# Kernel optimization log

Hardware: AMD Instinct MI355X
Metric: run time of the kernel (lower is better)

The kernel has to match this reference:

```python
import jax, jax.numpy as jnp
import numpy as np

HIDDEN = 2048
INPUT = 2048
BATCH = 4096


def setup_inputs() -> dict:
    key = jax.random.key(0)
    ks = jax.random.split(key, 7)
    x = jax.random.normal(ks[0], (BATCH, INPUT), dtype=jnp.float32)
    h = jax.random.normal(ks[1], (BATCH, HIDDEN), dtype=jnp.float32)
    c = jax.random.normal(ks[2], (BATCH, HIDDEN), dtype=jnp.float32)
    # learned parameters (RandomNormal init stddev=0.05 analogue; scale irrelevant for correctness)
    w_ih = jax.random.normal(ks[3], (4, INPUT, HIDDEN), dtype=jnp.float32) * 0.05
    w_hh = jax.random.normal(ks[4], (4, HIDDEN, HIDDEN), dtype=jnp.float32) * 0.05
    b_ih = jax.random.normal(ks[5], (4, HIDDEN), dtype=jnp.float32) * 0.05
    b_hh = jax.random.normal(ks[6], (4, HIDDEN), dtype=jnp.float32) * 0.05
    return {"x": x, "h": h, "c": c, "w_ih": w_ih, "w_hh": w_hh, "b_ih": b_ih, "b_hh": b_hh}


def reference(x, h, c, w_ih, w_hh, b_ih, b_hh):
    # gates: [4, B, H] = x @ w_ih[g] and h @ w_hh[g], batched over gate dim g
    gates = (
        jnp.einsum("bi,gih->gbh", x, w_ih)
        + jnp.einsum("bh,ghk->gbk", h, w_hh)
        + (b_ih + b_hh)[:, None, :]
    )
    ingate = jax.nn.sigmoid(gates[0])
    forgetgate = jax.nn.sigmoid(gates[1])
    cellgate = jnp.tanh(gates[2])
    outgate = jax.nn.sigmoid(gates[3])
    c_new = forgetgate * c + ingate * cellgate
    h_new = outgate * jnp.tanh(c_new)
    return (h_new, c_new)
```

## Files before the change

### kernel.cpp

```cpp
#include <hip/hip_runtime.h>

#define BATCH  4096
#define HIDDEN 2048
#define INPUT  2048
#define KDIM   4096
#define NDIM   8192
#define BM 256
#define BN 256
#define BK 64
#define NT (KDIM / BK)

typedef __attribute__((ext_vector_type(8))) short short8;
typedef __attribute__((ext_vector_type(4))) float float4v;


__device__ __forceinline__ unsigned short f2bf(float f) {
    union { float f; unsigned u; } v; v.f = f;
    unsigned r = v.u + 0x7FFFu + ((v.u >> 16) & 1u);
    return (unsigned short)(r >> 16);
}

__device__ __forceinline__ void gl2lds16(const unsigned short* g, unsigned short* l) {
    __builtin_amdgcn_global_load_lds(
        (const __attribute__((address_space(1))) unsigned int*)g,
        (__attribute__((address_space(3))) unsigned int*)l,
        16, 0, 0);
}

__device__ __forceinline__ float sigm(float x) {
    return 1.0f / (1.0f + __expf(-x));
}
__device__ __forceinline__ float tanh_fast(float x) {
    return 2.0f / (1.0f + __expf(-2.0f * x)) - 1.0f;
}

__device__ __forceinline__ void fence_bar() {
    asm volatile("" ::: "memory");
    __builtin_amdgcn_s_barrier();
    asm volatile("" ::: "memory");
}


__global__ void pack_x_kernel(const float* __restrict__ x, const float* __restrict__ h,
                              unsigned short* __restrict__ Xb) {
    int idx = blockIdx.x * 256 + threadIdx.x;
    int b  = idx >> 9;
    int ko = idx & 511;
    const float* src = (ko < 256) ? (x + (size_t)b * INPUT  + (size_t)ko * 8)
                                  : (h + (size_t)b * HIDDEN + (size_t)(ko - 256) * 8);
    float4 v0 = *(const float4*)(src);
    float4 v1 = *(const float4*)(src + 4);
    union { unsigned short us[8]; uint4 v; } o;
    o.us[0] = f2bf(v0.x); o.us[1] = f2bf(v0.y); o.us[2] = f2bf(v0.z); o.us[3] = f2bf(v0.w);
    o.us[4] = f2bf(v1.x); o.us[5] = f2bf(v1.y); o.us[6] = f2bf(v1.z); o.us[7] = f2bf(v1.w);
    *(uint4*)(Xb + (size_t)b * KDIM + (size_t)ko * 8) = o.v;
}


__global__ void pack_w_kernel(const float* __restrict__ w_ih, const float* __restrict__ w_hh,
                              unsigned short* __restrict__ Wt) {
    __shared__ unsigned short tile[32][136];
    const int k0 = blockIdx.x * 128;
    const int j0 = blockIdx.y * 32;
    const int g  = blockIdx.z;
    const float* src = (k0 < INPUT)
        ? (w_ih + (size_t)g * INPUT  * HIDDEN + (size_t)k0 * HIDDEN + j0)
        : (w_hh + (size_t)g * HIDDEN * HIDDEN + (size_t)(k0 - INPUT) * HIDDEN + j0);

    const int tid = threadIdx.x;
    const int jl  = (tid & 7) * 4;
    const int kl  = (tid >> 3) * 2;
#pragma unroll
    for (int p = 0; p < 2; ++p) {
        const int k = kl + p * 64;
        float4 v0 = *(const float4*)(src + (size_t)k * HIDDEN + jl);
        float4 v1 = *(const float4*)(src + (size_t)(k + 1) * HIDDEN + jl);
        unsigned p0 = (unsigned)f2bf(v0.x) | ((unsigned)f2bf(v1.x) << 16);
        unsigned p1 = (unsigned)f2bf(v0.y) | ((unsigned)f2bf(v1.y) << 16);
        unsigned p2 = (unsigned)f2bf(v0.z) | ((unsigned)f2bf(v1.z) << 16);
        unsigned p3 = (unsigned)f2bf(v0.w) | ((unsigned)f2bf(v1.w) << 16);
        *(unsigned*)&tile[jl + 0][k] = p0;
        *(unsigned*)&tile[jl + 1][k] = p1;
        *(unsigned*)&tile[jl + 2][k] = p2;
        *(unsigned*)&tile[jl + 3][k] = p3;
    }
    __syncthreads();

#pragma unroll
    for (int p = 0; p < 2; ++p) {
        const int cch = tid + p * 256;
        const int j   = cch >> 4;
        const int k8  = cch & 15;
        uint4 v = *(const uint4*)&tile[j][k8 * 8];
        *(uint4*)(Wt + (size_t)(4 * (j0 + j) + g) * KDIM + k0 + k8 * 8) = v;
    }
}


__global__ __launch_bounds__(512, 2)
void gemm_kernel(const unsigned short* __restrict__ A,
                 const unsigned short* __restrict__ B,
                 const float* __restrict__ c,
                 const float* __restrict__ b_ih,
                 const float* __restrict__ b_hh,
                 float* __restrict__ out) {
    extern __shared__ unsigned short lds[];
    unsigned short* cA = lds;
    unsigned short* nA = lds + 16384;
    unsigned short* cB = lds + 32768;
    unsigned short* nB = lds + 49152;

    const int tid  = threadIdx.x;
    const int wid  = tid >> 6;
    const int lane = tid & 63;
    const int ln   = lane & 15;
    const int kq   = lane >> 4;
    const int wmr  = (wid >> 2) * 128;
    const int wnr  = (wid & 3) * 64;
    const int m0   = blockIdx.y * BM;
    const int n0   = blockIdx.x * BN;

    const int srow  = tid >> 3;
    const int scol8 = (tid & 7) ^ (srow & 7);
    const unsigned short* gA[4];
    const unsigned short* gB[4];
#pragma unroll
    for (int cN = 0; cN < 4; ++cN) {
        gA[cN] = A + (size_t)(m0 + cN * 64 + srow) * KDIM + scol8 * 8;
        gB[cN] = B + (size_t)(n0 + cN * 64 + srow) * KDIM + scol8 * 8;
    }
    const int dOff = tid * 8;

    const int abase = (wmr + ln) * 64;
    const int bbase = (wnr + ln) * 64;
    const int sk0 = ((0 + kq) ^ (ln & 7)) * 8;
    const int sk1 = ((4 + kq) ^ (ln & 7)) * 8;

    float4v acc[8][4];
#pragma unroll
    for (int i = 0; i < 8; ++i)
#pragma unroll
        for (int j = 0; j < 4; ++j)
            acc[i][j] = (float4v){0.f, 0.f, 0.f, 0.f};

#define STAGE_A(cN) gl2lds16(gA[cN] + konext, nA + (cN) * 4096 + dOff)
#define STAGE_B(cN) gl2lds16(gB[cN] + konext, nB + (cN) * 4096 + dOff)

    {
        const int konext = 0;
        unsigned short* sA = cA; unsigned short* sB = cB;
#pragma unroll
        for (int cN = 0; cN < 4; ++cN) gl2lds16(gB[cN], sB + cN * 4096 + dOff);
#pragma unroll
        for (int cN = 0; cN < 4; ++cN) gl2lds16(gA[cN], sA + cN * 4096 + dOff);
        (void)konext;
    }

    short8 bf[4][2];

    for (int T = 0; T < NT; ++T) {
        const bool last = (T == NT - 1);
        const int konext = (T + 1) * BK;

        if (!last) { STAGE_B(0); STAGE_B(1); }
        if (!last) asm volatile("s_waitcnt vmcnt(2)" ::: "memory");
        else       asm volatile("s_waitcnt vmcnt(0)" ::: "memory");
        fence_bar();
        {
#pragma unroll
            for (int ni = 0; ni < 4; ++ni) {
                bf[ni][0] = *(const short8*)(cB + bbase + ni * 1024 + sk0);
                bf[ni][1] = *(const short8*)(cB + bbase + ni * 1024 + sk1);
            }
            short8 a00 = *(const short8*)(cA + abase + sk0);
            short8 a01 = *(const short8*)(cA + abase + sk1);
            short8 a10 = *(const short8*)(cA + abase + 1024 + sk0);
            short8 a11 = *(const short8*)(cA + abase + 1024 + sk1);
            __builtin_amdgcn_s_setprio(1);
#pragma unroll
            for (int ni = 0; ni < 4; ++ni)
                acc[0][ni] = __builtin_amdgcn_mfma_f32_16x16x32_bf16(a00, bf[ni][0], acc[0][ni], 0, 0, 0);
#pragma unroll
            for (int ni = 0; ni < 4; ++ni)
                acc[1][ni] = __builtin_amdgcn_mfma_f32_16x16x32_bf16(a10, bf[ni][0], acc[1][ni], 0, 0, 0);
#pragma unroll
            for (int ni = 0; ni < 4; ++ni)
                acc[0][ni] = __builtin_amdgcn_mfma_f32_16x16x32_bf16(a01, bf[ni][1], acc[0][ni], 0, 0, 0);
#pragma unroll
            for (int ni = 0; ni < 4; ++ni)
                acc[1][ni] = __builtin_amdgcn_mfma_f32_16x16x32_bf16(a11, bf[ni][1], acc[1][ni], 0, 0, 0);
            __builtin_amdgcn_s_setprio(0);
        }
        fence_bar();

#pragma unroll
        for (int ph = 1; ph < 4; ++ph) {
            if (!last) {
                if (ph == 1) { STAGE_B(2); STAGE_B(3); }
                if (ph == 2) { STAGE_A(0); STAGE_A(2); }
                if (ph == 3) { STAGE_A(1); STAGE_A(3); }
            }
            short8 a00 = *(const short8*)(cA + abase + (2 * ph) * 1024 + sk0);
            short8 a01 = *(const short8*)(cA + abase + (2 * ph) * 1024 + sk1);
            short8 a10 = *(const short8*)(cA + abase + (2 * ph + 1) * 1024 + sk0);
            short8 a11 = *(const short8*)(cA + abase + (2 * ph + 1) * 1024 + sk1);
            fence_bar();
            __builtin_amdgcn_s_setprio(1);
#pragma unroll
            for (int ni = 0; ni < 4; ++ni)
                acc[2 * ph][ni] = __builtin_amdgcn_mfma_f32_16x16x32_bf16(a00, bf[ni][0], acc[2 * ph][ni], 0, 0, 0);
#pragma unroll
            for (int ni = 0; ni < 4; ++ni)
                acc[2 * ph + 1][ni] = __builtin_amdgcn_mfma_f32_16x16x32_bf16(a10, bf[ni][0], acc[2 * ph + 1][ni], 0, 0, 0);
#pragma unroll
            for (int ni = 0; ni < 4; ++ni)
                acc[2 * ph][ni] = __builtin_amdgcn_mfma_f32_16x16x32_bf16(a01, bf[ni][1], acc[2 * ph][ni], 0, 0, 0);
#pragma unroll
            for (int ni = 0; ni < 4; ++ni)
                acc[2 * ph + 1][ni] = __builtin_amdgcn_mfma_f32_16x16x32_bf16(a11, bf[ni][1], acc[2 * ph + 1][ni], 0, 0, 0);
            __builtin_amdgcn_s_setprio(0);
            fence_bar();
        }

        unsigned short* t0 = cA; cA = nA; nA = t0;
        unsigned short* t1 = cB; cB = nB; nB = t1;
    }
#undef STAGE_A
#undef STAGE_B

    const int qg = lane & 3;
    const int t  = (lane & 15) >> 2;
    const size_t HB = (size_t)BATCH * HIDDEN;

#pragma unroll
    for (int ni = 0; ni < 4; ++ni) {
        const int jg = ((n0 + wnr + ni * 16) >> 2) + t;
        const float b0 = b_ih[jg]              + b_hh[jg];
        const float b1 = b_ih[HIDDEN + jg]     + b_hh[HIDDEN + jg];
        const float b2 = b_ih[2 * HIDDEN + jg] + b_hh[2 * HIDDEN + jg];
        const float b3 = b_ih[3 * HIDDEN + jg] + b_hh[3 * HIDDEN + jg];
#pragma unroll
        for (int mi = 0; mi < 8; ++mi) {
            float4v v = acc[mi][ni];
            float t1 = __shfl_xor((qg & 1) ? v[0] : v[1], 1);
            float t2 = __shfl_xor((qg & 1) ? v[2] : v[3], 1);
            v[0] = (qg & 1) ? t1 : v[0];
            v[1] = (qg & 1) ? v[1] : t1;
            v[2] = (qg & 1) ? t2 : v[2];
            v[3] = (qg & 1) ? v[3] : t2;
            float t3 = __shfl_xor((qg & 2) ? v[0] : v[2], 2);
            float t4 = __shfl_xor((qg & 2) ? v[1] : v[3], 2);
            v[0] = (qg & 2) ? t3 : v[0];
            v[1] = (qg & 2) ? t4 : v[1];
            v[2] = (qg & 2) ? v[2] : t3;
            v[3] = (qg & 2) ? v[3] : t4;

            const int row = m0 + wmr + mi * 16 + kq * 4 + qg;
            const float ig = sigm(v[0] + b0);
            const float fg = sigm(v[1] + b1);
            const float cg = tanh_fast(v[2] + b2);
            const float og = sigm(v[3] + b3);
            const float cv = c[(size_t)row * HIDDEN + jg];
            const float cn = fg * cv + ig * cg;
            const float hn = og * tanh_fast(cn);
            out[(size_t)row * HIDDEN + jg] = hn;
            out[HB + (size_t)row * HIDDEN + jg] = cn;
        }
    }
}


extern "C" void kernel_launch(void* const* d_in, const int* in_sizes, int n_in,
                              void* d_out, int out_size, void* d_ws, size_t ws_size,
                              hipStream_t stream) {
    const float* x    = (const float*)d_in[0];
    const float* h    = (const float*)d_in[1];
    const float* c    = (const float*)d_in[2];
    const float* w_ih = (const float*)d_in[3];
    const float* w_hh = (const float*)d_in[4];
    const float* b_ih = (const float*)d_in[5];
    const float* b_hh = (const float*)d_in[6];
    float* out = (float*)d_out;

    const size_t XB_BYTES = (size_t)BATCH * KDIM * 2;
    unsigned short* Xb = (unsigned short*)d_ws;
    unsigned short* Wt = (unsigned short*)((char*)d_ws + XB_BYTES);

    hipLaunchKernelGGL(pack_x_kernel, dim3((size_t)BATCH * KDIM / 8 / 256), dim3(256), 0, stream,
                       x, h, Xb);
    hipLaunchKernelGGL(pack_w_kernel, dim3(KDIM / 128, HIDDEN / 32, 4), dim3(256), 0, stream,
                       w_ih, w_hh, Wt);
    hipLaunchKernelGGL(gemm_kernel, dim3(NDIM / BN, BATCH / BM), dim3(512), 131072, stream,
                       Xb, Wt, c, b_ih, b_hh, out);
}
```

Before: 512.7 us.

## Issue all next-tile loads upfront and vectorize LSTM epilogue via lane transposes

```diff
diff --git a/kernel.cpp b/kernel.cpp
--- a/kernel.cpp
+++ b/kernel.cpp
@@ -79,10 +79,10 @@
         unsigned p1 = (unsigned)f2bf(v0.y) | ((unsigned)f2bf(v1.y) << 16);
         unsigned p2 = (unsigned)f2bf(v0.z) | ((unsigned)f2bf(v1.z) << 16);
         unsigned p3 = (unsigned)f2bf(v0.w) | ((unsigned)f2bf(v1.w) << 16);
-        *(unsigned*)&tile[jl + 0][k] = p0;
-        *(unsigned*)&tile[jl + 1][k] = p1;
-        *(unsigned*)&tile[jl + 2][k] = p2;
-        *(unsigned*)&tile[jl + 3][k] = p3;
+        *(unsigned*)&tile[jl + 0][kl + p * 64] = p0;
+        *(unsigned*)&tile[jl + 1][kl + p * 64] = p1;
+        *(unsigned*)&tile[jl + 2][kl + p * 64] = p2;
+        *(unsigned*)&tile[jl + 3][kl + p * 64] = p3;
     }
     __syncthreads();
 
@@ -147,13 +147,10 @@
 #define STAGE_B(cN) gl2lds16(gB[cN] + konext, nB + (cN) * 4096 + dOff)
 
     {
-        const int konext = 0;
-        unsigned short* sA = cA; unsigned short* sB = cB;
-#pragma unroll
-        for (int cN = 0; cN < 4; ++cN) gl2lds16(gB[cN], sB + cN * 4096 + dOff);
-#pragma unroll
-        for (int cN = 0; cN < 4; ++cN) gl2lds16(gA[cN], sA + cN * 4096 + dOff);
-        (void)konext;
+#pragma unroll
+        for (int cN = 0; cN < 4; ++cN) gl2lds16(gB[cN], cB + cN * 4096 + dOff);
+#pragma unroll
+        for (int cN = 0; cN < 4; ++cN) gl2lds16(gA[cN], cA + cN * 4096 + dOff);
     }
 
     short8 bf[4][2];
@@ -162,9 +159,13 @@
         const bool last = (T == NT - 1);
         const int konext = (T + 1) * BK;
 
-        if (!last) { STAGE_B(0); STAGE_B(1); }
-        if (!last) asm volatile("s_waitcnt vmcnt(2)" ::: "memory");
-        else       asm volatile("s_waitcnt vmcnt(0)" ::: "memory");
+        if (!last) {
+            STAGE_B(0); STAGE_B(1); STAGE_B(2); STAGE_B(3);
+            STAGE_A(0); STAGE_A(1); STAGE_A(2); STAGE_A(3);
+            asm volatile("s_waitcnt vmcnt(8)" ::: "memory");
+        } else {
+            asm volatile("s_waitcnt vmcnt(0)" ::: "memory");
+        }
         fence_bar();
         {
 #pragma unroll
@@ -195,11 +196,6 @@
 
 #pragma unroll
         for (int ph = 1; ph < 4; ++ph) {
-            if (!last) {
-                if (ph == 1) { STAGE_B(2); STAGE_B(3); }
-                if (ph == 2) { STAGE_A(0); STAGE_A(2); }
-                if (ph == 3) { STAGE_A(1); STAGE_A(3); }
-            }
             short8 a00 = *(const short8*)(cA + abase + (2 * ph) * 1024 + sk0);
             short8 a01 = *(const short8*)(cA + abase + (2 * ph) * 1024 + sk1);
             short8 a10 = *(const short8*)(cA + abase + (2 * ph + 1) * 1024 + sk0);
@@ -229,18 +225,25 @@
 #undef STAGE_B
 
     const int qg = lane & 3;
-    const int t  = (lane & 15) >> 2;
+    const int tq = (lane & 15) >> 2;
+    const int jb = (n0 >> 2) + (wnr >> 2);
     const size_t HB = (size_t)BATCH * HIDDEN;
 
+    float bia[4][4];
 #pragma unroll
     for (int ni = 0; ni < 4; ++ni) {
-        const int jg = ((n0 + wnr + ni * 16) >> 2) + t;
-        const float b0 = b_ih[jg]              + b_hh[jg];
-        const float b1 = b_ih[HIDDEN + jg]     + b_hh[HIDDEN + jg];
-        const float b2 = b_ih[2 * HIDDEN + jg] + b_hh[2 * HIDDEN + jg];
-        const float b3 = b_ih[3 * HIDDEN + jg] + b_hh[3 * HIDDEN + jg];
-#pragma unroll
-        for (int mi = 0; mi < 8; ++mi) {
+        const int jgq = jb + ni * 4 + tq;
+        bia[ni][0] = b_ih[jgq]              + b_hh[jgq];
+        bia[ni][1] = b_ih[HIDDEN + jgq]     + b_hh[HIDDEN + jgq];
+        bia[ni][2] = b_ih[2 * HIDDEN + jgq] + b_hh[2 * HIDDEN + jgq];
+        bia[ni][3] = b_ih[3 * HIDDEN + jgq] + b_hh[3 * HIDDEN + jgq];
+    }
+
+#pragma unroll
+    for (int mi = 0; mi < 8; ++mi) {
+        float fgv[4], pv[4], ogv[4];
+#pragma unroll
+        for (int ni = 0; ni < 4; ++ni) {
             float4v v = acc[mi][ni];
             float t1 = __shfl_xor((qg & 1) ? v[0] : v[1], 1);
             float t2 = __shfl_xor((qg & 1) ? v[2] : v[3], 1);
@@ -255,17 +258,51 @@
             v[2] = (qg & 2) ? v[2] : t3;
             v[3] = (qg & 2) ? v[3] : t4;
 
-            const int row = m0 + wmr + mi * 16 + kq * 4 + qg;
-            const float ig = sigm(v[0] + b0);
-            const float fg = sigm(v[1] + b1);
-            const float cg = tanh_fast(v[2] + b2);
-            const float og = sigm(v[3] + b3);
-            const float cv = c[(size_t)row * HIDDEN + jg];
-            const float cn = fg * cv + ig * cg;
-            const float hn = og * tanh_fast(cn);
-            out[(size_t)row * HIDDEN + jg] = hn;
-            out[HB + (size_t)row * HIDDEN + jg] = cn;
-        }
+            const float ig = sigm(v[0] + bia[ni][0]);
+            const float fg = sigm(v[1] + bia[ni][1]);
+            const float cg = tanh_fast(v[2] + bia[ni][2]);
+            const float og = sigm(v[3] + bia[ni][3]);
+            fgv[ni] = fg;
+            pv[ni]  = ig * cg;
+            ogv[ni] = og;
+        }
+#define TRANS_T(a)                                                        \
+        {                                                                 \
+            float u1 = __shfl_xor((tq & 1) ? a[0] : a[1], 4);             \
+            float u2 = __shfl_xor((tq & 1) ? a[2] : a[3], 4);             \
+            a[0] = (tq & 1) ? u1 : a[0];                                  \
+            a[1] = (tq & 1) ? a[1] : u1;                                  \
+            a[2] = (tq & 1) ? u2 : a[2];                                  \
+            a[3] = (tq & 1) ? a[3] : u2;                                  \
+            float u3 = __shfl_xor((tq & 2) ? a[0] : a[2], 8);             \
+            float u4 = __shfl_xor((tq & 2) ? a[1] : a[3], 8);             \
+            a[0] = (tq & 2) ? u3 : a[0];                                  \
+            a[2] = (tq & 2) ? a[2] : u3;                                  \
+            a[1] = (tq & 2) ? u4 : a[1];                                  \
+            a[3] = (tq & 2) ? a[3] : u4;                                  \
+        }
+        TRANS_T(fgv);
+        TRANS_T(pv);
+        TRANS_T(ogv);
+#undef TRANS_T
+
+        const int row = m0 + wmr + mi * 16 + kq * 4 + qg;
+        const int jcol = jb + 4 * tq;
+        const float4 cv = *(const float4*)(c + (size_t)row * HIDDEN + jcol);
+        float4 hn4, cn4;
+        {
+            const float cn0 = fgv[0] * cv.x + pv[0];
+            const float cn1 = fgv[1] * cv.y + pv[1];
+            const float cn2 = fgv[2] * cv.z + pv[2];
+            const float cn3 = fgv[3] * cv.w + pv[3];
+            cn4.x = cn0; cn4.y = cn1; cn4.z = cn2; cn4.w = cn3;
+            hn4.x = ogv[0] * tanh_fast(cn0);
+            hn4.y = ogv[1] * tanh_fast(cn1);
+            hn4.z = ogv[2] * tanh_fast(cn2);
+            hn4.w = ogv[3] * tanh_fast(cn3);
+        }
+        *(float4*)(out + (size_t)row * HIDDEN + jcol)      = hn4;
+        *(float4*)(out + HB + (size_t)row * HIDDEN + jcol) = cn4;
     }
 }
 
```

Result: faster. 487.4 us (-4.9%).
